# Performance work log

Measured on AMD Instinct MI355X. Metric: run time of the kernel, lower is better.

## Reference

```python
import jax, jax.numpy as jnp
import numpy as np

B, H, N, L = 8, 128, 64, 8192
LOG_DT_MIN, LOG_DT_MAX = float(np.log(0.001)), float(np.log(0.1))


def setup_inputs() -> dict:
    key = jax.random.key(0)
    k_x, k_are, k_aim, k_c, k_dt = jax.random.split(key, 5)
    x = jax.random.normal(k_x, (B, H, L), dtype=jnp.float32)
    # A_re: negative real parts (clipped to <= -1e-4 in forward anyway)
    A_re = -jax.random.uniform(k_are, (H, N, 1), dtype=jnp.float32, minval=0.1, maxval=1.0)
    A_im = jax.random.normal(k_aim, (H, N, 1), dtype=jnp.float32) * float(np.pi)
    C = (0.5 ** 0.5) * jax.random.normal(k_c, (H, N, 2), dtype=jnp.float32)
    D = jnp.ones((1, H, 1), dtype=jnp.float32)
    u = jax.random.uniform(k_dt, (H, 1, 1), dtype=jnp.float32)
    log_delta = u * (LOG_DT_MAX - LOG_DT_MIN) + LOG_DT_MIN
    return {"x": x, "A_re": A_re, "A_im": A_im, "C": C, "D": D, "log_delta": log_delta}


def reference(x, A_re, A_im, C, D, log_delta):
    seq_len = x.shape[-1]
    # ---- S4D-ZOH kernel generation ----
    A = jnp.minimum(A_re, -1e-4) + 1j * A_im            # (H, N, 1) complex
    Cc = C[..., 0:1] + 1j * C[..., 1:2]                 # (H, N, 1) complex
    step = jnp.exp(log_delta)                           # (H, 1, 1)
    dA = step * A                                       # (H, N, 1)
    times = jnp.arange(seq_len, dtype=jnp.float32)[None, None, :]  # (1, 1, L)
    part = jnp.exp(times * dA)                          # (H, N, L)
    cons = (jnp.exp(dA) - 1.0) / A                      # (H, N, 1)
    K = jnp.sum(Cc * cons * part, axis=-2).real         # (H, L)
    # ---- causal conv via FFT (torch pads both to length 2L) ----
    n = seq_len + K.shape[-1]                           # 2L
    xd = jnp.fft.rfft(x, n=n, axis=-1)                  # (B, H, L+1)
    Kd = jnp.fft.rfft(K[None], n=n, axis=-1)            # (1, H, L+1)
    conv = jnp.fft.irfft(xd * Kd, n=n, axis=-1)[:, :, :seq_len]
    return conv + D * x
```

## Files before the change

kernel.cpp:

```cpp
#include <hip/hip_runtime.h>
#include <hip/hip_bf16.h>
#include <math.h>

#define B_ 8
#define H_ 128
#define N_ 64
#define L_ 8192
#define MCH 64
#define SCH (L_ / MCH)
#define EROW 136

typedef __attribute__((ext_vector_type(8))) short bf16x8;
typedef __attribute__((ext_vector_type(4))) float f32x4;

__device__ __forceinline__ float bf2f(ushort s) { return __uint_as_float(((uint)s) << 16); }
__device__ __forceinline__ uint packbf2(float a, float b) {
    __hip_bfloat162 h = __float22bfloat162_rn(make_float2(a, b));
    union { __hip_bfloat162 h2; uint u; } cv; cv.h2 = h;
    return cv.u;
}
__device__ __forceinline__ bf16x8 pack_bf8(f32x4 a, f32x4 b) {
    union { uint u[4]; bf16x8 v; } r;
    r.u[0] = packbf2(a[0], a[1]); r.u[1] = packbf2(a[2], a[3]);
    r.u[2] = packbf2(b[0], b[1]); r.u[3] = packbf2(b[2], b[3]);
    return r.v;
}

__global__ __launch_bounds__(256) void s4d_build(
    const float* __restrict__ A_re, const float* __restrict__ A_im,
    const float* __restrict__ C, const float* __restrict__ D,
    const float* __restrict__ log_delta,
    ushort* __restrict__ wsT, ushort* __restrict__ wsP,
    ushort* __restrict__ wsQ, float2* __restrict__ wsRM)
{
    __shared__ float kpart[64][65];
    __shared__ float kv[64];
    __shared__ uint  pbuf[32 * 68];

    const int h = blockIdx.x >> 1;
    const int e = blockIdx.x & 1;
    const int tid = threadIdx.x;
    const int n = tid & 63;
    const int g = tid >> 6;

    float are = fminf(A_re[h * N_ + n], -1e-4f);
    float aim = A_im[h * N_ + n];
    float step = expf(log_delta[h]);
    float dre = step * are, dim = step * aim;
    float er = expf(dre);
    float sd, cd; sincosf(dim, &sd, &cd);
    float rre = er * cd;
    float rim = er * sd;
    float cre = C[(h * N_ + n) * 2 + 0];
    float cim = C[(h * N_ + n) * 2 + 1];
    float inv  = 1.0f / (are * are + aim * aim);
    float numr = rre - 1.0f, numi = rim;
    float consr = (numr * are + numi * aim) * inv;
    float consi = (numi * are - numr * aim) * inv;
    float wr = cre * consr - cim * consi;
    float wi = cre * consi + cim * consr;
    float dval = D[h];

    auto rp = [&](float d, float& pr, float& pi) {
        float ex = __expf(d * dre);
        float ang = d * dim;
        float s = __sinf(ang), c2 = __cosf(ang);
        pr = ex * c2; pi = ex * s;
    };

#pragma unroll
    for (int j = 0; j < 16; ++j) {
        int d = g * 16 + j;
        float pr, pi; rp((float)d, pr, pi);
        kpart[d][n] = wr * pr - wi * pi;
    }
    __syncthreads();
    if (tid < 64) {
        float s = 0.f;
#pragma unroll
        for (int m = 0; m < 64; ++m) s += kpart[tid][m];
        kv[tid] = s;
    }
    __syncthreads();

    {
        uint tw[4];
#pragma unroll
        for (int i = 0; i < 4; ++i) {
            int t0 = e * 32 + g * 8 + 2 * i, t1 = t0 + 1;
            float v0 = (t0 <= n) ? kv[n - t0] : 0.f;
            float v1 = (t1 <= n) ? kv[n - t1] : 0.f;
            if (t0 == n) v0 += dval;
            if (t1 == n) v1 += dval;
            tw[i] = packbf2(v0, v1);
        }
        *(uint4*)(wsT + ((size_t)h * 64 + n) * 64 + e * 32 + g * 8) = *(uint4*)tw;
    }

    {
        uint qr[4], qi[4];
#pragma unroll
        for (int i = 0; i < 4; ++i) {
            int t0 = e * 32 + g * 8 + 2 * i;
            float ar0, ai0, ar1, ai1;
            rp((float)(63 - t0), ar0, ai0);
            rp((float)(62 - t0), ar1, ai1);
            qr[i] = packbf2(ar0, ar1);
            qi[i] = packbf2(ai0, ai1);
        }
        *(uint4*)(wsQ + ((size_t)h * 128 + 2 * n    ) * 64 + e * 32 + g * 8) = *(uint4*)qr;
        *(uint4*)(wsQ + ((size_t)h * 128 + 2 * n + 1) * 64 + e * 32 + g * 8) = *(uint4*)qi;
    }

#pragma unroll
    for (int i = 0; i < 8; ++i) {
        int jl = g * 8 + i;
        int j = e * 32 + jl;
        float pr, pi; rp((float)(j + 1), pr, pi);
        float ur = wr * pr - wi * pi;
        float ui = wr * pi + wi * pr;
        pbuf[jl * 68 + n] = packbf2(ur, -ui);
    }
    if (tid < 64) {
        float mr = rre, mi = rim;
#pragma unroll
        for (int k = 0; k < 6; ++k) { float tr = mr*mr - mi*mi, ti = 2.f*mr*mi; mr = tr; mi = ti; }
        wsRM[h * 64 + n] = make_float2(mr, mi);
    }
    __syncthreads();
    {
        const int rw = tid & 31, cc = tid >> 5;
        const uint* src = &pbuf[rw * 68 + cc * 8];
        uint4* dP = (uint4*)(wsP + ((size_t)h * 64 + e * 32 + rw) * 128 + cc * 16);
        dP[0] = *(const uint4*)(src);
        dP[1] = *(const uint4*)(src + 4);
    }
}

__global__ __launch_bounds__(256, 4) void s4d_main(
    const float* __restrict__ x,
    const ushort* __restrict__ wsT, const ushort* __restrict__ wsP,
    const ushort* __restrict__ wsQ, const float2* __restrict__ wsRM,
    float* __restrict__ out)
{
    __shared__ ushort EBUF[SCH * EROW];
    __shared__ float segr[4][64], segi[4][64];

    const int seq = blockIdx.x;
    const int h   = seq % H_;
    const int tid = threadIdx.x;
    const int w   = tid >> 6;
    const int lane = tid & 63;
    const int n16 = lane & 15, q = lane >> 4;

    const float* xs = x + (size_t)seq * L_;

    bf16x8 xb[2][2];
#pragma unroll
    for (int ic = 0; ic < 2; ++ic) {
        int c = (2 * w + ic) * 16 + n16;
#pragma unroll
        for (int kc = 0; kc < 2; ++kc) {
            const float* p = xs + c * MCH + kc * 32 + q * 8;
            f32x4 f0 = __builtin_nontemporal_load((const f32x4*)p);
            f32x4 f1 = __builtin_nontemporal_load((const f32x4*)p + 1);
            xb[ic][kc] = pack_bf8(f0, f1);
        }
    }

    const ushort* Qh = wsQ + (size_t)h * 128 * 64;
#pragma unroll
    for (int rt = 0; rt < 8; ++rt) {
        bf16x8 a0 = *(const bf16x8*)(Qh + ((size_t)(rt * 16 + n16)) * 64 +      q * 8);
        bf16x8 a1 = *(const bf16x8*)(Qh + ((size_t)(rt * 16 + n16)) * 64 + 32 + q * 8);
#pragma unroll
        for (int ic = 0; ic < 2; ++ic) {
            f32x4 acc = {0.f, 0.f, 0.f, 0.f};
            acc = __builtin_amdgcn_mfma_f32_16x16x32_bf16(a0, xb[ic][0], acc, 0, 0, 0);
            acc = __builtin_amdgcn_mfma_f32_16x16x32_bf16(a1, xb[ic][1], acc, 0, 0, 0);
            int c = (2 * w + ic) * 16 + n16;
            uint2 st = make_uint2(packbf2(acc[0], acc[1]), packbf2(acc[2], acc[3]));
            *(uint2*)&EBUF[c * EROW + rt * 16 + q * 4] = st;
        }
    }

    const ushort* Th = wsT + (size_t)h * 64 * 64;
    f32x4 accT[4][2];
#pragma unroll
    for (int rt = 0; rt < 4; ++rt) {
        bf16x8 t0 = *(const bf16x8*)(Th + ((size_t)(rt * 16 + n16)) * 64 +      q * 8);
        bf16x8 t1 = *(const bf16x8*)(Th + ((size_t)(rt * 16 + n16)) * 64 + 32 + q * 8);
#pragma unroll
        for (int ic = 0; ic < 2; ++ic) {
            f32x4 a = {0.f, 0.f, 0.f, 0.f};
            a = __builtin_amdgcn_mfma_f32_16x16x32_bf16(t0, xb[ic][0], a, 0, 0, 0);
            a = __builtin_amdgcn_mfma_f32_16x16x32_bf16(t1, xb[ic][1], a, 0, 0, 0);
            accT[rt][ic] = a;
        }
    }
    __syncthreads();

    {
        const int nB = tid & 63, gB = tid >> 6;
        float2 rm = wsRM[h * 64 + nB];
        float mr = rm.x, mi = rm.y;
        float m32r = mr, m32i = mi;
#pragma unroll
        for (int k = 0; k < 5; ++k) {
            float tr = m32r * m32r - m32i * m32i, ti = 2.f * m32r * m32i;
            m32r = tr; m32i = ti;
        }
        float sr = 0.f, si = 0.f;
#pragma unroll
        for (int j = 0; j < 32; ++j) {
            uint e = *(const uint*)&EBUF[(gB * 32 + j) * EROW + 2 * nB];
            float er2 = bf2f((ushort)(e & 0xffffu)), ei2 = bf2f((ushort)(e >> 16));
            float nr = er2 + mr * sr - mi * si;
            float ni = ei2 + mr * si + mi * sr;
            sr = nr; si = ni;
        }
        segr[gB][nB] = sr; segi[gB][nB] = si;
        __syncthreads();
        float pr2 = 0.f, pi2 = 0.f;
        for (int gp = 0; gp < gB; ++gp) {
            float Er = segr[gp][nB], Ei = segi[gp][nB];
            float nr = Er + m32r * pr2 - m32i * pi2;
            float ni = Ei + m32r * pi2 + m32i * pr2;
            pr2 = nr; pi2 = ni;
        }
        sr = pr2; si = pi2;
#pragma unroll
        for (int j = 0; j < 32; ++j) {
            uint* ep = (uint*)&EBUF[(gB * 32 + j) * EROW + 2 * nB];
            uint e = *ep;
            float er2 = bf2f((ushort)(e & 0xffffu)), ei2 = bf2f((ushort)(e >> 16));
            *ep = packbf2(sr, si);
            float nr = er2 + mr * sr - mi * si;
            float ni = ei2 + mr * si + mi * sr;
            sr = nr; si = ni;
        }
    }

    const ushort* Ph = wsP + (size_t)h * 64 * 128;
    bf16x8 pf0 = *(const bf16x8*)(Ph + (size_t)n16 * 128 +       q * 8);
    bf16x8 pf1 = *(const bf16x8*)(Ph + (size_t)n16 * 128 +  32 + q * 8);
    bf16x8 pf2 = *(const bf16x8*)(Ph + (size_t)n16 * 128 +  64 + q * 8);
    bf16x8 pf3 = *(const bf16x8*)(Ph + (size_t)n16 * 128 +  96 + q * 8);
    __syncthreads();

    float* op = out + (size_t)seq * L_;
#pragma unroll
    for (int rt = 0; rt < 4; ++rt) {
        bf16x8 p0, p1, p2, p3;
        if (rt == 0) { p0 = pf0; p1 = pf1; p2 = pf2; p3 = pf3; }
        else {
            p0 = *(const bf16x8*)(Ph + ((size_t)(rt * 16 + n16)) * 128 +       q * 8);
            p1 = *(const bf16x8*)(Ph + ((size_t)(rt * 16 + n16)) * 128 +  32 + q * 8);
            p2 = *(const bf16x8*)(Ph + ((size_t)(rt * 16 + n16)) * 128 +  64 + q * 8);
            p3 = *(const bf16x8*)(Ph + ((size_t)(rt * 16 + n16)) * 128 +  96 + q * 8);
        }
#pragma unroll
        for (int ic = 0; ic < 2; ++ic) {
            int c = (2 * w + ic) * 16 + n16;
            f32x4 accP = {0.f, 0.f, 0.f, 0.f};
            accP = __builtin_amdgcn_mfma_f32_16x16x32_bf16(p0,
                       *(const bf16x8*)&EBUF[c * EROW +       q * 8], accP, 0, 0, 0);
            accP = __builtin_amdgcn_mfma_f32_16x16x32_bf16(p1,
                       *(const bf16x8*)&EBUF[c * EROW +  32 + q * 8], accP, 0, 0, 0);
            accP = __builtin_amdgcn_mfma_f32_16x16x32_bf16(p2,
                       *(const bf16x8*)&EBUF[c * EROW +  64 + q * 8], accP, 0, 0, 0);
            accP = __builtin_amdgcn_mfma_f32_16x16x32_bf16(p3,
                       *(const bf16x8*)&EBUF[c * EROW +  96 + q * 8], accP, 0, 0, 0);
            f32x4 o;
            o[0] = accT[rt][ic][0] + accP[0];
            o[1] = accT[rt][ic][1] + accP[1];
            o[2] = accT[rt][ic][2] + accP[2];
            o[3] = accT[rt][ic][3] + accP[3];
            __builtin_nontemporal_store(o, (f32x4*)(op + c * MCH + rt * 16 + q * 4));
        }
    }
}

extern "C" void kernel_launch(void* const* d_in, const int* in_sizes, int n_in,
                              void* d_out, int out_size, void* d_ws, size_t ws_size,
                              hipStream_t stream)
{
    const float* x  = (const float*)d_in[0];
    const float* Ar = (const float*)d_in[1];
    const float* Ai = (const float*)d_in[2];
    const float* C  = (const float*)d_in[3];
    const float* D  = (const float*)d_in[4];
    const float* ld = (const float*)d_in[5];
    float* out = (float*)d_out;

    ushort* wsT = (ushort*)d_ws;
    ushort* wsP = wsT + (size_t)128 * 64 * 64;
    ushort* wsQ = wsP + (size_t)128 * 64 * 128;
    float2* wsRM = (float2*)(wsQ + (size_t)128 * 128 * 64);

    hipLaunchKernelGGL(s4d_build, dim3(H_ * 2), dim3(256), 0, stream,
                       Ar, Ai, C, D, ld, wsT, wsP, wsQ, wsRM);
    hipLaunchKernelGGL(s4d_main, dim3(B_ * H_), dim3(256), 0, stream,
                       x, wsT, wsP, wsQ, wsRM, out);
}
```

Measured before the change: 115.4 us.

## Fuse S4D kernel-table build into main kernel using swizzled LDS tables

Merges the separate build kernel into the main per-sequence kernel. Each block now recomputes the Toeplitz, Q and P tables for its head directly into XOR-swizzled shared memory, so it no longer reads them from a global workspace and saves a kernel launch. In exchange each table is recomputed once per batch element (8x redundant transcendental work), LDS grows to about 53KB, and the occupancy hint drops from 4 to 3 blocks.

```diff
diff --git a/kernel.cpp b/kernel.cpp
--- a/kernel.cpp
+++ b/kernel.cpp
@@ -10,6 +10,11 @@
 #define SCH (L_ / MCH)
 #define EROW 136
 
+#define LDS_TBL   34816
+#define LDS_SEG   51200
+#define LDS_KV    53248
+#define LDS_TOTAL 53504
+
 typedef __attribute__((ext_vector_type(8))) short bf16x8;
 typedef __attribute__((ext_vector_type(4))) float f32x4;
 
@@ -26,20 +31,27 @@
     return r.v;
 }
 
-__global__ __launch_bounds__(256) void s4d_build(
+__global__ __launch_bounds__(256, 3) void s4d_fused(
+    const float* __restrict__ x,
     const float* __restrict__ A_re, const float* __restrict__ A_im,
-    const float* __restrict__ C, const float* __restrict__ D,
+    const float* __restrict__ Cp, const float* __restrict__ Dp,
     const float* __restrict__ log_delta,
-    ushort* __restrict__ wsT, ushort* __restrict__ wsP,
-    ushort* __restrict__ wsQ, float2* __restrict__ wsRM)
+    float* __restrict__ out)
 {
-    __shared__ float kpart[64][65];
-    __shared__ float kv[64];
-    __shared__ uint  pbuf[32 * 68];
-
-    const int h = blockIdx.x >> 1;
-    const int e = blockIdx.x & 1;
+    __shared__ __align__(16) char lds[LDS_TOTAL];
+    ushort* EBUF  = (ushort*)lds;
+    float*  kpart = (float*)lds;
+    char*   TBLb  = lds + LDS_TBL;
+    float*  segr  = (float*)(lds + LDS_SEG);
+    float*  segi  = segr + 256;
+    float*  kv    = (float*)(lds + LDS_KV);
+
+    const int seq = blockIdx.x;
+    const int h   = seq % H_;
     const int tid = threadIdx.x;
+    const int w   = tid >> 6;
+    const int lane = tid & 63;
+    const int n16 = lane & 15, q = lane >> 4;
     const int n = tid & 63;
     const int g = tid >> 6;
 
@@ -49,17 +61,19 @@
     float dre = step * are, dim = step * aim;
     float er = expf(dre);
     float sd, cd; sincosf(dim, &sd, &cd);
-    float rre = er * cd;
-    float rim = er * sd;
-    float cre = C[(h * N_ + n) * 2 + 0];
-    float cim = C[(h * N_ + n) * 2 + 1];
+    float rre = er * cd, rim = er * sd;
+    float cre = Cp[(h * N_ + n) * 2 + 0];
+    float cim = Cp[(h * N_ + n) * 2 + 1];
     float inv  = 1.0f / (are * are + aim * aim);
     float numr = rre - 1.0f, numi = rim;
     float consr = (numr * are + numi * aim) * inv;
     float consi = (numi * are - numr * aim) * inv;
     float wr = cre * consr - cim * consi;
     float wi = cre * consi + cim * consr;
-    float dval = D[h];
+    float dval = Dp[h];
+    float m64r = rre, m64i = rim;
+#pragma unroll
+    for (int k = 0; k < 6; ++k) { float tr = m64r*m64r - m64i*m64i, ti = 2.f*m64r*m64i; m64r = tr; m64i = ti; }
 
     auto rp = [&](float d, float& pr, float& pi) {
         float ex = __expf(d * dre);
@@ -68,170 +82,148 @@
         pr = ex * c2; pi = ex * s;
     };
 
+    const float* xs = x + (size_t)seq * L_;
+    bf16x8 xbv[2][2];
+#pragma unroll
+    for (int ic = 0; ic < 2; ++ic) {
+        int c = (2 * w + ic) * 16 + n16;
+#pragma unroll
+        for (int kc = 0; kc < 2; ++kc) {
+            const float* p = xs + c * MCH + kc * 32 + q * 8;
+            f32x4 f0 = __builtin_nontemporal_load((const f32x4*)p);
+            f32x4 f1 = __builtin_nontemporal_load((const f32x4*)p + 1);
+            xbv[ic][kc] = pack_bf8(f0, f1);
+        }
+    }
+
 #pragma unroll
     for (int j = 0; j < 16; ++j) {
         int d = g * 16 + j;
         float pr, pi; rp((float)d, pr, pi);
-        kpart[d][n] = wr * pr - wi * pi;
+        kpart[d * 65 + n] = wr * pr - wi * pi;
     }
     __syncthreads();
     if (tid < 64) {
         float s = 0.f;
 #pragma unroll
-        for (int m = 0; m < 64; ++m) s += kpart[tid][m];
+        for (int m = 0; m < 64; ++m) s += kpart[tid * 65 + m];
         kv[tid] = s;
     }
     __syncthreads();
 
     {
-        uint tw[4];
-#pragma unroll
-        for (int i = 0; i < 4; ++i) {
-            int t0 = e * 32 + g * 8 + 2 * i, t1 = t0 + 1;
+        uint tw[8];
+#pragma unroll
+        for (int i = 0; i < 8; ++i) {
+            int t0 = g * 16 + 2 * i, t1 = t0 + 1;
             float v0 = (t0 <= n) ? kv[n - t0] : 0.f;
             float v1 = (t1 <= n) ? kv[n - t1] : 0.f;
             if (t0 == n) v0 += dval;
             if (t1 == n) v1 += dval;
             tw[i] = packbf2(v0, v1);
         }
-        *(uint4*)(wsT + ((size_t)h * 64 + n) * 64 + e * 32 + g * 8) = *(uint4*)tw;
-    }
-
-    {
-        uint qr[4], qi[4];
-#pragma unroll
-        for (int i = 0; i < 4; ++i) {
-            int t0 = e * 32 + g * 8 + 2 * i;
+        const uint xt = (uint)(n & 7) << 4;
+        *(uint4*)(TBLb + ((n * 128 + g * 32     ) ^ xt)) = ((uint4*)tw)[0];
+        *(uint4*)(TBLb + ((n * 128 + g * 32 + 16) ^ xt)) = ((uint4*)tw)[1];
+    }
+    __syncthreads();
+
+    const uint xr = (uint)(n16 & 7) << 4;
+    f32x4 accT[4][2];
+#pragma unroll
+    for (int rt = 0; rt < 4; ++rt) {
+        int row = rt * 16 + n16;
+        bf16x8 t0 = *(const bf16x8*)(TBLb + ((row * 128      + q * 16) ^ xr));
+        bf16x8 t1 = *(const bf16x8*)(TBLb + ((row * 128 + 64 + q * 16) ^ xr));
+#pragma unroll
+        for (int ic = 0; ic < 2; ++ic) {
+            f32x4 a = {0.f, 0.f, 0.f, 0.f};
+            a = __builtin_amdgcn_mfma_f32_16x16x32_bf16(t0, xbv[ic][0], a, 0, 0, 0);
+            a = __builtin_amdgcn_mfma_f32_16x16x32_bf16(t1, xbv[ic][1], a, 0, 0, 0);
+            accT[rt][ic] = a;
+        }
+    }
+    __syncthreads();
+
+    {
+        uint qr[8], qi[8];
+#pragma unroll
+        for (int i = 0; i < 8; ++i) {
+            int t0 = g * 16 + 2 * i;
             float ar0, ai0, ar1, ai1;
             rp((float)(63 - t0), ar0, ai0);
             rp((float)(62 - t0), ar1, ai1);
             qr[i] = packbf2(ar0, ar1);
             qi[i] = packbf2(ai0, ai1);
         }
-        *(uint4*)(wsQ + ((size_t)h * 128 + 2 * n    ) * 64 + e * 32 + g * 8) = *(uint4*)qr;
-        *(uint4*)(wsQ + ((size_t)h * 128 + 2 * n + 1) * 64 + e * 32 + g * 8) = *(uint4*)qi;
-    }
-
-#pragma unroll
-    for (int i = 0; i < 8; ++i) {
-        int jl = g * 8 + i;
-        int j = e * 32 + jl;
-        float pr, pi; rp((float)(j + 1), pr, pi);
-        float ur = wr * pr - wi * pi;
-        float ui = wr * pi + wi * pr;
-        pbuf[jl * 68 + n] = packbf2(ur, -ui);
-    }
-    if (tid < 64) {
-        float mr = rre, mi = rim;
-#pragma unroll
-        for (int k = 0; k < 6; ++k) { float tr = mr*mr - mi*mi, ti = 2.f*mr*mi; mr = tr; mi = ti; }
-        wsRM[h * 64 + n] = make_float2(mr, mi);
-    }
-    __syncthreads();
-    {
-        const int rw = tid & 31, cc = tid >> 5;
-        const uint* src = &pbuf[rw * 68 + cc * 8];
-        uint4* dP = (uint4*)(wsP + ((size_t)h * 64 + e * 32 + rw) * 128 + cc * 16);
-        dP[0] = *(const uint4*)(src);
-        dP[1] = *(const uint4*)(src + 4);
-    }
-}
-
-__global__ __launch_bounds__(256, 4) void s4d_main(
-    const float* __restrict__ x,
-    const ushort* __restrict__ wsT, const ushort* __restrict__ wsP,
-    const ushort* __restrict__ wsQ, const float2* __restrict__ wsRM,
-    float* __restrict__ out)
-{
-    __shared__ ushort EBUF[SCH * EROW];
-    __shared__ float segr[4][64], segi[4][64];
-
-    const int seq = blockIdx.x;
-    const int h   = seq % H_;
-    const int tid = threadIdx.x;
-    const int w   = tid >> 6;
-    const int lane = tid & 63;
-    const int n16 = lane & 15, q = lane >> 4;
-
-    const float* xs = x + (size_t)seq * L_;
-
-    bf16x8 xb[2][2];
-#pragma unroll
-    for (int ic = 0; ic < 2; ++ic) {
-        int c = (2 * w + ic) * 16 + n16;
-#pragma unroll
-        for (int kc = 0; kc < 2; ++kc) {
-            const float* p = xs + c * MCH + kc * 32 + q * 8;
-            f32x4 f0 = __builtin_nontemporal_load((const f32x4*)p);
-            f32x4 f1 = __builtin_nontemporal_load((const f32x4*)p + 1);
-            xb[ic][kc] = pack_bf8(f0, f1);
-        }
-    }
-
-    const ushort* Qh = wsQ + (size_t)h * 128 * 64;
+        const int ra = 2 * n, rb = 2 * n + 1;
+        const uint xa = (uint)(ra & 7) << 4, xbm = (uint)(rb & 7) << 4;
+        *(uint4*)(TBLb + ((ra * 128 + g * 32     ) ^ xa)) = ((uint4*)qr)[0];
+        *(uint4*)(TBLb + ((ra * 128 + g * 32 + 16) ^ xa)) = ((uint4*)qr)[1];
+        *(uint4*)(TBLb + ((rb * 128 + g * 32     ) ^ xbm)) = ((uint4*)qi)[0];
+        *(uint4*)(TBLb + ((rb * 128 + g * 32 + 16) ^ xbm)) = ((uint4*)qi)[1];
+    }
+    __syncthreads();
+
 #pragma unroll
     for (int rt = 0; rt < 8; ++rt) {
-        bf16x8 a0 = *(const bf16x8*)(Qh + ((size_t)(rt * 16 + n16)) * 64 +      q * 8);
-        bf16x8 a1 = *(const bf16x8*)(Qh + ((size_t)(rt * 16 + n16)) * 64 + 32 + q * 8);
+        int row = rt * 16 + n16;
+        bf16x8 a0 = *(const bf16x8*)(TBLb + ((row * 128      + q * 16) ^ xr));
+        bf16x8 a1 = *(const bf16x8*)(TBLb + ((row * 128 + 64 + q * 16) ^ xr));
 #pragma unroll
         for (int ic = 0; ic < 2; ++ic) {
             f32x4 acc = {0.f, 0.f, 0.f, 0.f};
-            acc = __builtin_amdgcn_mfma_f32_16x16x32_bf16(a0, xb[ic][0], acc, 0, 0, 0);
-            acc = __builtin_amdgcn_mfma_f32_16x16x32_bf16(a1, xb[ic][1], acc, 0, 0, 0);
+            acc = __builtin_amdgcn_mfma_f32_16x16x32_bf16(a0, xbv[ic][0], acc, 0, 0, 0);
+            acc = __builtin_amdgcn_mfma_f32_16x16x32_bf16(a1, xbv[ic][1], acc, 0, 0, 0);
             int c = (2 * w + ic) * 16 + n16;
             uint2 st = make_uint2(packbf2(acc[0], acc[1]), packbf2(acc[2], acc[3]));
             *(uint2*)&EBUF[c * EROW + rt * 16 + q * 4] = st;
         }
     }
-
-    const ushort* Th = wsT + (size_t)h * 64 * 64;
-    f32x4 accT[4][2];
-#pragma unroll
-    for (int rt = 0; rt < 4; ++rt) {
-        bf16x8 t0 = *(const bf16x8*)(Th + ((size_t)(rt * 16 + n16)) * 64 +      q * 8);
-        bf16x8 t1 = *(const bf16x8*)(Th + ((size_t)(rt * 16 + n16)) * 64 + 32 + q * 8);
-#pragma unroll
-        for (int ic = 0; ic < 2; ++ic) {
-            f32x4 a = {0.f, 0.f, 0.f, 0.f};
-            a = __builtin_amdgcn_mfma_f32_16x16x32_bf16(t0, xb[ic][0], a, 0, 0, 0);
-            a = __builtin_amdgcn_mfma_f32_16x16x32_bf16(t1, xb[ic][1], a, 0, 0, 0);
-            accT[rt][ic] = a;
-        }
-    }
-    __syncthreads();
-
-    {
-        const int nB = tid & 63, gB = tid >> 6;
-        float2 rm = wsRM[h * 64 + nB];
-        float mr = rm.x, mi = rm.y;
-        float m32r = mr, m32i = mi;
-#pragma unroll
-        for (int k = 0; k < 5; ++k) {
-            float tr = m32r * m32r - m32i * m32i, ti = 2.f * m32r * m32i;
-            m32r = tr; m32i = ti;
-        }
+    __syncthreads();
+
+    float mr = m64r, mi = m64i;
+    float m32r = mr, m32i = mi;
+#pragma unroll
+    for (int k = 0; k < 5; ++k) {
+        float tr = m32r * m32r - m32i * m32i, ti = 2.f * m32r * m32i;
+        m32r = tr; m32i = ti;
+    }
+    {
         float sr = 0.f, si = 0.f;
 #pragma unroll
         for (int j = 0; j < 32; ++j) {
-            uint e = *(const uint*)&EBUF[(gB * 32 + j) * EROW + 2 * nB];
+            uint e = *(const uint*)&EBUF[(g * 32 + j) * EROW + 2 * n];
             float er2 = bf2f((ushort)(e & 0xffffu)), ei2 = bf2f((ushort)(e >> 16));
             float nr = er2 + mr * sr - mi * si;
             float ni = ei2 + mr * si + mi * sr;
             sr = nr; si = ni;
         }
-        segr[gB][nB] = sr; segi[gB][nB] = si;
-        __syncthreads();
+        segr[g * 64 + n] = sr; segi[g * 64 + n] = si;
+    }
+    {
+#pragma unroll
+        for (int i = 0; i < 16; ++i) {
+            int j = g * 16 + i;
+            float pr, pi; rp((float)(j + 1), pr, pi);
+            float ur = wr * pr - wi * pi;
+            float ui = wr * pi + wi * pr;
+            *(uint*)(TBLb + ((j * 256 + n * 4) ^ ((uint)(j & 7) << 4))) = packbf2(ur, -ui);
+        }
+    }
+    __syncthreads();
+    {
         float pr2 = 0.f, pi2 = 0.f;
-        for (int gp = 0; gp < gB; ++gp) {
-            float Er = segr[gp][nB], Ei = segi[gp][nB];
+        for (int gp = 0; gp < g; ++gp) {
+            float Er = segr[gp * 64 + n], Ei = segi[gp * 64 + n];
             float nr = Er + m32r * pr2 - m32i * pi2;
             float ni = Ei + m32r * pi2 + m32i * pr2;
             pr2 = nr; pi2 = ni;
         }
-        sr = pr2; si = pi2;
+        float sr = pr2, si = pi2;
 #pragma unroll
         for (int j = 0; j < 32; ++j) {
-            uint* ep = (uint*)&EBUF[(gB * 32 + j) * EROW + 2 * nB];
+            uint* ep = (uint*)&EBUF[(g * 32 + j) * EROW + 2 * n];
             uint e = *ep;
             float er2 = bf2f((ushort)(e & 0xffffu)), ei2 = bf2f((ushort)(e >> 16));
             *ep = packbf2(sr, si);
@@ -240,25 +232,16 @@
             sr = nr; si = ni;
         }
     }
-
-    const ushort* Ph = wsP + (size_t)h * 64 * 128;
-    bf16x8 pf0 = *(const bf16x8*)(Ph + (size_t)n16 * 128 +       q * 8);
-    bf16x8 pf1 = *(const bf16x8*)(Ph + (size_t)n16 * 128 +  32 + q * 8);
-    bf16x8 pf2 = *(const bf16x8*)(Ph + (size_t)n16 * 128 +  64 + q * 8);
-    bf16x8 pf3 = *(const bf16x8*)(Ph + (size_t)n16 * 128 +  96 + q * 8);
     __syncthreads();
 
     float* op = out + (size_t)seq * L_;
 #pragma unroll
     for (int rt = 0; rt < 4; ++rt) {
-        bf16x8 p0, p1, p2, p3;
-        if (rt == 0) { p0 = pf0; p1 = pf1; p2 = pf2; p3 = pf3; }
-        else {
-            p0 = *(const bf16x8*)(Ph + ((size_t)(rt * 16 + n16)) * 128 +       q * 8);
-            p1 = *(const bf16x8*)(Ph + ((size_t)(rt * 16 + n16)) * 128 +  32 + q * 8);
-            p2 = *(const bf16x8*)(Ph + ((size_t)(rt * 16 + n16)) * 128 +  64 + q * 8);
-            p3 = *(const bf16x8*)(Ph + ((size_t)(rt * 16 + n16)) * 128 +  96 + q * 8);
-        }
+        int row = rt * 16 + n16;
+        bf16x8 p0 = *(const bf16x8*)(TBLb + ((row * 256       + q * 16) ^ xr));
+        bf16x8 p1 = *(const bf16x8*)(TBLb + ((row * 256 +  64 + q * 16) ^ xr));
+        bf16x8 p2 = *(const bf16x8*)(TBLb + ((row * 256 + 128 + q * 16) ^ xr));
+        bf16x8 p3 = *(const bf16x8*)(TBLb + ((row * 256 + 192 + q * 16) ^ xr));
 #pragma unroll
         for (int ic = 0; ic < 2; ++ic) {
             int c = (2 * w + ic) * 16 + n16;
@@ -292,14 +275,8 @@
     const float* D  = (const float*)d_in[4];
     const float* ld = (const float*)d_in[5];
     float* out = (float*)d_out;
-
-    ushort* wsT = (ushort*)d_ws;
-    ushort* wsP = wsT + (size_t)128 * 64 * 64;
-    ushort* wsQ = wsP + (size_t)128 * 64 * 128;
-    float2* wsRM = (float2*)(wsQ + (size_t)128 * 128 * 64);
-
-    hipLaunchKernelGGL(s4d_build, dim3(H_ * 2), dim3(256), 0, stream,
-                       Ar, Ai, C, D, ld, wsT, wsP, wsQ, wsRM);
-    hipLaunchKernelGGL(s4d_main, dim3(B_ * H_), dim3(256), 0, stream,
-                       x, wsT, wsP, wsQ, wsRM, out);
-}
+    (void)d_ws; (void)ws_size;
+
+    hipLaunchKernelGGL(s4d_fused, dim3(B_ * H_), dim3(256), 0, stream,
+                       x, Ar, Ai, C, D, ld, out);
+}
```

New measurement: 112.9 us. 1.02x faster.
